# Optimization experiments

Measured on AMD Instinct MI355X. Metric: run time of the kernel, lower is better.

The kernel has to match this reference:

```python
import jax, jax.numpy as jnp
import numpy as np
import math

H = 16          # num_attention_heads
DH = 64         # attention_head_size
D = H * DH      # hidden_size
MAXPOS = 512    # max_position_embeddings
ALPHA = 12.0
MAX_SEQ = 512
GAMMA = -ALPHA / MAX_SEQ
ETA = 1.0


def setup_inputs() -> dict:
    key = jax.random.key(0)
    ks = jax.random.split(key, 10)
    B, S = 16, 512
    s = 1.0 / math.sqrt(D)
    return {
        "hidden_states": jax.random.normal(ks[0], (B, S, D), jnp.float32),
        "attention_mask": jnp.zeros((B, 1, 1, S), jnp.float32),
        "Wq": jax.random.normal(ks[1], (D, D), jnp.float32) * s,
        "bq": jnp.zeros((D,), jnp.float32),
        "Wk": jax.random.normal(ks[2], (D, D), jnp.float32) * s,
        "bk": jnp.zeros((D,), jnp.float32),
        "Wv": jax.random.normal(ks[3], (D, D), jnp.float32) * s,
        "bv": jnp.zeros((D,), jnp.float32),
        "dist_emb": jax.random.normal(ks[4], (2 * MAXPOS - 1, DH), jnp.float32) * 0.02,
        "gate_w": jax.random.normal(ks[5], (H, DH), jnp.float32) * 0.01,
        "gate_b": jnp.zeros((H,), jnp.float32),
    }


def _heads(x, B, S):
    # [B,S,D] -> [B,H,S,DH]
    return x.reshape(B, S, H, DH).transpose(0, 2, 1, 3)


def reference(hidden_states, attention_mask, Wq, bq, Wk, bk, Wv, bv,
              dist_emb, gate_w, gate_b):
    B, S, _ = hidden_states.shape
    q = _heads(hidden_states @ Wq + bq, B, S)  # bhsd
    k = _heads(hidden_states @ Wk + bk, B, S)
    v = _heads(hidden_states @ Wv + bv, B, S)

    scores = jnp.einsum("bhqd,bhkd->bhqk", q, k)

    # relative_key_query positional scores
    pos = jnp.arange(S)
    distance = pos[:, None] - pos[None, :]          # [S,S]
    pe = dist_emb[distance + MAXPOS - 1]            # [S,S,DH]
    scores = scores + jnp.einsum("bhld,lrd->bhlr", q, pe) \
                    + jnp.einsum("bhrd,lrd->bhlr", k, pe)

    scores = scores / math.sqrt(DH) + attention_mask

    # clipped softmax: clip((eta-gamma)*softmax(x) + gamma, 0, 1)
    probs = jnp.clip(jax.nn.softmax(scores, axis=-1) * (ETA - GAMMA) + GAMMA,
                     0.0, 1.0)

    ctx = jnp.einsum("bhqk,bhkd->bhqd", probs, v)

    # conditional_per_token per-head gate: sigmoid(Linear(head_dim -> 1))
    x_heads = _heads(hidden_states, B, S)            # bhsd
    gate = jax.nn.sigmoid(
        jnp.einsum("bhsd,hd->bhs", x_heads, gate_w) + gate_b[None, :, None])
    ctx = ctx * gate[..., None]

    return ctx.transpose(0, 2, 1, 3).reshape(B, S, D)
```

## Files before the change

kernel.cpp:

```cpp
#include <hip/hip_runtime.h>

typedef __attribute__((ext_vector_type(8))) short s16x8;
typedef __attribute__((ext_vector_type(4))) short s16x4;
typedef __attribute__((ext_vector_type(4))) float f32x4;

__device__ __forceinline__ f32x4 mfma16(s16x8 a, s16x8 b, f32x4 c) {
  return __builtin_amdgcn_mfma_f32_16x16x32_bf16(a, b, c, 0, 0, 0);
}
__device__ __forceinline__ f32x4 zero4() {
  f32x4 z = {0.f, 0.f, 0.f, 0.f};
  return z;
}

__device__ __forceinline__ unsigned short f2b(float f) {
  unsigned u = __float_as_uint(f);
  u = u + 0x7fffu + ((u >> 16) & 1u);
  return (unsigned short)(u >> 16);
}
__device__ __forceinline__ float b2f(unsigned short u) {
  return __uint_as_float(((unsigned)u) << 16);
}
__device__ __forceinline__ unsigned packbf(float a, float b) {
  return (unsigned)f2b(a) | ((unsigned)f2b(b) << 16);
}


__global__ __launch_bounds__(256) void k0a_convx_gate(
    const float* __restrict__ X, const float* __restrict__ gw,
    const float* __restrict__ gb, unsigned short* __restrict__ Xb,
    float* __restrict__ gate) {
  int row = blockIdx.x;
  int t = threadIdx.x;
  const float* xr = X + (size_t)row * 1024;
  float4 x = *(const float4*)(xr + t * 4);
  s16x4 o;
  o.x = (short)f2b(x.x); o.y = (short)f2b(x.y);
  o.z = (short)f2b(x.z); o.w = (short)f2b(x.w);
  *(s16x4*)(&Xb[(size_t)row * 1024 + t * 4]) = o;
  int h = t >> 4;
  int e0 = (t & 15) * 4;
  const float* g4 = gw + h * 64 + e0;
  float part = x.x * g4[0] + x.y * g4[1] + x.z * g4[2] + x.w * g4[3];
  part += __shfl_xor(part, 1);
  part += __shfl_xor(part, 2);
  part += __shfl_xor(part, 4);
  part += __shfl_xor(part, 8);
  if ((t & 15) == 0) {
    int b = row >> 9, s = row & 511;
    float z = part + gb[h];
    gate[((size_t)(b * 16 + h)) * 512 + s] = 1.0f / (1.0f + __expf(-z));
  }
}

__global__ __launch_bounds__(256) void k0b_wtrans(
    const float* __restrict__ Wq, const float* __restrict__ Wk,
    const float* __restrict__ Wv, unsigned short* __restrict__ Wt) {
  __shared__ float tile[64][68];
  int z = blockIdx.z;
  const float* W = (z == 0) ? Wq : (z == 1) ? Wk : Wv;
  unsigned short* O = Wt + (size_t)z * 1024 * 1024;
  int k0 = blockIdx.x * 64, n0 = blockIdx.y * 64;
  int t = threadIdx.x;
  int kl = t >> 4, nl = (t & 15) * 4;
#pragma unroll
  for (int p = 0; p < 4; ++p) {
    float4 v = *(const float4*)(W + (size_t)(k0 + p * 16 + kl) * 1024 + n0 + nl);
    tile[p * 16 + kl][nl + 0] = v.x;
    tile[p * 16 + kl][nl + 1] = v.y;
    tile[p * 16 + kl][nl + 2] = v.z;
    tile[p * 16 + kl][nl + 3] = v.w;
  }
  __syncthreads();
  for (int idx = t; idx < 4096; idx += 256) {
    int nl2 = idx >> 6, kl2 = idx & 63;
    O[(size_t)(n0 + nl2) * 1024 + k0 + kl2] = f2b(tile[kl2][nl2]);
  }
}

__global__ __launch_bounds__(256) void k0c_conve(const float* __restrict__ E,
                                                 unsigned short* __restrict__ Eb) {
  int idx = blockIdx.x * 256 + threadIdx.x;
  int row = idx >> 6;
  float v = (row < 1023) ? E[idx] : 0.0f;
  Eb[idx] = f2b(v);
}

__global__ __launch_bounds__(256) void k1_qkv(
    const unsigned short* __restrict__ Xb, const unsigned short* __restrict__ Wt,
    const float* __restrict__ bq, const float* __restrict__ bk,
    const float* __restrict__ bv, unsigned short* __restrict__ Qb,
    unsigned short* __restrict__ Kb, unsigned short* __restrict__ Vt) {
  __shared__ short As[128 * 72];
  __shared__ short Ws[128 * 72];
  int t = threadIdx.x;
  int wv = t >> 6, lane = t & 63, quad = lane >> 4, l15 = lane & 15;
  int wm = wv >> 1, wn = wv & 1;
  int m0 = blockIdx.x * 128, n0 = blockIdx.y * 128, z = blockIdx.z;
  const unsigned short* W = Wt + (size_t)z * 1024 * 1024;
  f32x4 acc[4][4];
#pragma unroll
  for (int i = 0; i < 4; ++i)
#pragma unroll
    for (int j = 0; j < 4; ++j) acc[i][j] = zero4();

  for (int kt = 0; kt < 16; ++kt) {
    int k0 = kt * 64;
    __syncthreads();
#pragma unroll
    for (int p = 0; p < 4; ++p) {
      int g = p * 256 + t;
      int row = g >> 3, cg = g & 7;
      int4 va = *(const int4*)(Xb + (size_t)(m0 + row) * 1024 + k0 + cg * 8);
      *(int4*)(&As[row * 72 + cg * 8]) = va;
      int4 vb = *(const int4*)(W + (size_t)(n0 + row) * 1024 + k0 + cg * 8);
      *(int4*)(&Ws[row * 72 + cg * 8]) = vb;
    }
    __syncthreads();
#pragma unroll
    for (int ks = 0; ks < 2; ++ks) {
      s16x8 a[4], bb[4];
#pragma unroll
      for (int i = 0; i < 4; ++i)
        a[i] = *(const s16x8*)(&As[(wm * 64 + i * 16 + l15) * 72 + ks * 32 + quad * 8]);
#pragma unroll
      for (int j = 0; j < 4; ++j)
        bb[j] = *(const s16x8*)(&Ws[(wn * 64 + j * 16 + l15) * 72 + ks * 32 + quad * 8]);
#pragma unroll
      for (int i = 0; i < 4; ++i)
#pragma unroll
        for (int j = 0; j < 4; ++j)
          acc[i][j] = mfma16(a[i], bb[j], acc[i][j]);
    }
  }
  const float* bias = (z == 0) ? bq : (z == 1) ? bk : bv;
#pragma unroll
  for (int i = 0; i < 4; ++i) {
    int mbase = m0 + wm * 64 + i * 16 + quad * 4;
#pragma unroll
    for (int j = 0; j < 4; ++j) {
      int n = n0 + wn * 64 + j * 16 + l15;
      float bvv = bias[n];
      int h = n >> 6, dh = n & 63;
#pragma unroll
      for (int r = 0; r < 4; ++r) {
        int m = mbase + r;
        int b = m >> 9, s = m & 511;
        unsigned short u = f2b(acc[i][j][r] + bvv);
        if (z == 2)
          Vt[(size_t)((b * 16 + h) * 64 + dh) * 512 + s] = u;
        else if (z == 0)
          Qb[(size_t)((b * 16 + h) * 512 + s) * 64 + dh] = u;
        else
          Kb[(size_t)((b * 16 + h) * 512 + s) * 64 + dh] = u;
      }
    }
  }
}

__global__ __launch_bounds__(256, 3) void k2_attn(
    const unsigned short* __restrict__ Qb, const unsigned short* __restrict__ Kb,
    const unsigned short* __restrict__ Vt, const unsigned short* __restrict__ Eb,
    const float* __restrict__ gate, const float* __restrict__ mask,
    float* __restrict__ out) {
  __shared__ short Ks[64 * 72];
  __shared__ short Ss1[128 * 68];
  __shared__ short Ss2[128 * 68];
  __shared__ short Ps[64 * 72];

  int t = threadIdx.x;
  int wv = t >> 6, lane = t & 63, quad = lane >> 4, l15 = lane & 15;
  int bid = blockIdx.x;
  int bh = bid >> 3, qt = bid & 7;
  int b = bh >> 4, hh = bh & 15;
  int l0 = qt * 64;

  int srow = t >> 3, scg = t & 7;

  s16x8 aq0, aq1;
  {
    const unsigned short* qp = Qb + ((size_t)bh * 512 + l0 + wv * 16 + l15) * 64 + quad * 8;
    aq0 = *(const s16x8*)(qp);
    aq1 = *(const s16x8*)(qp + 32);
  }

  float lsum[4];
#pragma unroll
  for (int r = 0; r < 4; ++r) lsum[r] = 0.0f;
  unsigned stash[64];

#pragma unroll
  for (int kt = 0; kt < 8; ++kt) {
    int r0 = kt * 64;
    int4 kv0 = *(const int4*)(Kb + ((size_t)bh * 512 + r0 + srow) * 64 + scg * 8);
    int4 kv1 = *(const int4*)(Kb + ((size_t)bh * 512 + r0 + srow + 32) * 64 + scg * 8);
    __syncthreads();
    *(int4*)(&Ks[srow * 72 + scg * 8]) = kv0;
    *(int4*)(&Ks[(srow + 32) * 72 + scg * 8]) = kv1;
    __syncthreads();
    s16x8 ak0 = *(const s16x8*)(&Ks[(wv * 16 + l15) * 72 + quad * 8]);
    s16x8 ak1 = *(const s16x8*)(&Ks[(wv * 16 + l15) * 72 + 32 + quad * 8]);
    int estart = (qt - kt) * 64 + 448;
#pragma unroll
    for (int nf = 0; nf < 8; ++nf) {
      const s16x8* ep = (const s16x8*)(Eb + (size_t)(estart + nf * 16 + l15) * 64 + quad * 8);
      s16x8 eb0 = ep[0];
      s16x8 eb1 = ep[4];
      f32x4 s1 = mfma16(aq1, eb1, mfma16(aq0, eb0, zero4()));
      s16x4 w1;
      w1.x = (short)f2b(s1[0]); w1.y = (short)f2b(s1[1]);
      w1.z = (short)f2b(s1[2]); w1.w = (short)f2b(s1[3]);
      *(s16x4*)(&Ss1[(nf * 16 + l15) * 68 + wv * 16 + quad * 4]) = w1;
      f32x4 s2 = mfma16(ak1, eb1, mfma16(ak0, eb0, zero4()));
      s16x4 w2;
      w2.x = (short)f2b(s2[0]); w2.y = (short)f2b(s2[1]);
      w2.z = (short)f2b(s2[2]); w2.w = (short)f2b(s2[3]);
      *(s16x4*)(&Ss2[(nf * 16 + l15) * 68 + wv * 16 + quad * 4]) = w2;
    }
    f32x4 s[4];
#pragma unroll
    for (int nf = 0; nf < 4; ++nf) {
      s16x8 b0 = *(const s16x8*)(&Ks[(nf * 16 + l15) * 72 + quad * 8]);
      s16x8 b1 = *(const s16x8*)(&Ks[(nf * 16 + l15) * 72 + 32 + quad * 8]);
      s[nf] = mfma16(aq1, b1, mfma16(aq0, b0, zero4()));
    }
    __syncthreads();
#pragma unroll
    for (int nf = 0; nf < 4; ++nf) {
      float mkv = mask[b * 512 + kt * 64 + nf * 16 + l15];
      int dr = nf * 16 + l15;
      float ex[4];
#pragma unroll
      for (int r = 0; r < 4; ++r) {
        int dl = wv * 16 + quad * 4 + r;
        int tt = dl - dr + 63;
        float p1 = b2f((unsigned short)Ss1[tt * 68 + dl]);
        float p2 = b2f((unsigned short)Ss2[tt * 68 + dr]);
        float x = (s[nf][r] + p1 + p2) * 0.125f + mkv;
        ex[r] = __expf(x);
        lsum[r] += ex[r];
      }
      stash[kt * 8 + nf * 2 + 0] = packbf(ex[0], ex[1]);
      stash[kt * 8 + nf * 2 + 1] = packbf(ex[2], ex[3]);
    }
  }

#pragma unroll
  for (int r = 0; r < 4; ++r) {
    lsum[r] += __shfl_xor(lsum[r], 1);
    lsum[r] += __shfl_xor(lsum[r], 2);
    lsum[r] += __shfl_xor(lsum[r], 4);
    lsum[r] += __shfl_xor(lsum[r], 8);
  }
  float f1[4];
#pragma unroll
  for (int r = 0; r < 4; ++r) f1[r] = 1.0234375f / lsum[r];
  const float c0 = -0.0234375f;

  f32x4 ctx[4];
#pragma unroll
  for (int nf = 0; nf < 4; ++nf) ctx[nf] = zero4();

#pragma unroll
  for (int kt = 0; kt < 8; ++kt) {
#pragma unroll
    for (int nf = 0; nf < 4; ++nf) {
      unsigned u0 = stash[kt * 8 + nf * 2 + 0];
      unsigned u1 = stash[kt * 8 + nf * 2 + 1];
      float e0 = b2f((unsigned short)(u0 & 0xffff));
      float e1 = b2f((unsigned short)(u0 >> 16));
      float e2 = b2f((unsigned short)(u1 & 0xffff));
      float e3 = b2f((unsigned short)(u1 >> 16));
      float p0 = fminf(fmaxf(e0 * f1[0] + c0, 0.0f), 1.0f);
      float p1 = fminf(fmaxf(e1 * f1[1] + c0, 0.0f), 1.0f);
      float p2 = fminf(fmaxf(e2 * f1[2] + c0, 0.0f), 1.0f);
      float p3 = fminf(fmaxf(e3 * f1[3] + c0, 0.0f), 1.0f);
      int rowb = wv * 16 + quad * 4;
      Ps[(rowb + 0) * 72 + nf * 16 + l15] = (short)f2b(p0);
      Ps[(rowb + 1) * 72 + nf * 16 + l15] = (short)f2b(p1);
      Ps[(rowb + 2) * 72 + nf * 16 + l15] = (short)f2b(p2);
      Ps[(rowb + 3) * 72 + nf * 16 + l15] = (short)f2b(p3);
    }
    s16x8 ap0 = *(const s16x8*)(&Ps[(wv * 16 + l15) * 72 + quad * 8]);
    s16x8 ap1 = *(const s16x8*)(&Ps[(wv * 16 + l15) * 72 + 32 + quad * 8]);
#pragma unroll
    for (int nf = 0; nf < 4; ++nf) {
      const s16x8* vp = (const s16x8*)(Vt + ((size_t)bh * 64 + nf * 16 + l15) * 512 + kt * 64 + quad * 8);
      s16x8 vb0 = vp[0];
      s16x8 vb1 = vp[4];
      ctx[nf] = mfma16(ap1, vb1, mfma16(ap0, vb0, ctx[nf]));
    }
  }

#pragma unroll
  for (int r = 0; r < 4; ++r) {
    int s = l0 + wv * 16 + quad * 4 + r;
    float g = gate[(size_t)bh * 512 + s];
#pragma unroll
    for (int nf = 0; nf < 4; ++nf)
      out[((size_t)(b * 512 + s)) * 1024 + hh * 64 + nf * 16 + l15] = ctx[nf][r] * g;
  }
}

extern "C" void kernel_launch(void* const* d_in, const int* in_sizes, int n_in,
                              void* d_out, int out_size, void* d_ws, size_t ws_size,
                              hipStream_t stream) {
  const float* X = (const float*)d_in[0];
  const float* mask = (const float*)d_in[1];
  const float* Wq = (const float*)d_in[2];
  const float* bq = (const float*)d_in[3];
  const float* Wk = (const float*)d_in[4];
  const float* bk = (const float*)d_in[5];
  const float* Wv = (const float*)d_in[6];
  const float* bv = (const float*)d_in[7];
  const float* dist = (const float*)d_in[8];
  const float* gw = (const float*)d_in[9];
  const float* gb = (const float*)d_in[10];
  float* out = (float*)d_out;

  char* ws = (char*)d_ws;
  constexpr size_t OFF_XB = 0;
  constexpr size_t OFF_WT = 16777216;
  constexpr size_t OFF_QB = OFF_WT + 6291456;
  constexpr size_t OFF_KB = OFF_QB + 16777216;
  constexpr size_t OFF_VT = OFF_KB + 16777216;
  constexpr size_t OFF_EB = OFF_VT + 16777216;
  constexpr size_t OFF_GA = OFF_EB + 131072;

  unsigned short* Xb = (unsigned short*)(ws + OFF_XB);
  unsigned short* Wt = (unsigned short*)(ws + OFF_WT);
  unsigned short* Qb = (unsigned short*)(ws + OFF_QB);
  unsigned short* Kb = (unsigned short*)(ws + OFF_KB);
  unsigned short* Vt = (unsigned short*)(ws + OFF_VT);
  unsigned short* Eb = (unsigned short*)(ws + OFF_EB);
  float* gate = (float*)(ws + OFF_GA);

  hipLaunchKernelGGL(k0a_convx_gate, dim3(8192), dim3(256), 0, stream, X, gw, gb, Xb, gate);
  hipLaunchKernelGGL(k0b_wtrans, dim3(16, 16, 3), dim3(256), 0, stream, Wq, Wk, Wv, Wt);
  hipLaunchKernelGGL(k0c_conve, dim3(256), dim3(256), 0, stream, dist, Eb);
  hipLaunchKernelGGL(k1_qkv, dim3(64, 8, 3), dim3(256), 0, stream,
                     Xb, Wt, bq, bk, bv, Qb, Kb, Vt);
  hipLaunchKernelGGL(k2_attn, dim3(2048), dim3(256), 0, stream,
                     Qb, Kb, Vt, Eb, gate, mask, out);
}
```

Measured before the change: 406.9 us.

## Use direct global-to-LDS loads in QKV GEMM and drop K staging in attention

Result: slower. 471.1 us (+15.8%).

```diff
diff --git a/kernel.cpp b/kernel.cpp
--- a/kernel.cpp
+++ b/kernel.cpp
@@ -22,6 +22,12 @@
 }
 __device__ __forceinline__ unsigned packbf(float a, float b) {
   return (unsigned)f2b(a) | ((unsigned)f2b(b) << 16);
+}
+
+__device__ __forceinline__ void gld16(const void* g, void* l) {
+  __builtin_amdgcn_global_load_lds(
+      (const __attribute__((address_space(1))) void*)g,
+      (__attribute__((address_space(3))) void*)l, 16, 0, 0);
 }
 
 
@@ -90,30 +96,31 @@
     const float* __restrict__ bq, const float* __restrict__ bk,
     const float* __restrict__ bv, unsigned short* __restrict__ Qb,
     unsigned short* __restrict__ Kb, unsigned short* __restrict__ Vt) {
-  __shared__ short As[128 * 72];
-  __shared__ short Ws[128 * 72];
+  __shared__ short As[128 * 64];
+  __shared__ short Ws[128 * 64];
   int t = threadIdx.x;
   int wv = t >> 6, lane = t & 63, quad = lane >> 4, l15 = lane & 15;
   int wm = wv >> 1, wn = wv & 1;
-  int m0 = blockIdx.x * 128, n0 = blockIdx.y * 128, z = blockIdx.z;
+  int bx = blockIdx.x;
+  bx = ((bx & 7) << 3) | (bx >> 3);
+  int m0 = bx * 128, n0 = blockIdx.y * 128, z = blockIdx.z;
   const unsigned short* W = Wt + (size_t)z * 1024 * 1024;
   f32x4 acc[4][4];
 #pragma unroll
   for (int i = 0; i < 4; ++i)
 #pragma unroll
     for (int j = 0; j < 4; ++j) acc[i][j] = zero4();
+
+  int srow = t >> 3, scg = t & 7;
 
   for (int kt = 0; kt < 16; ++kt) {
     int k0 = kt * 64;
     __syncthreads();
 #pragma unroll
     for (int p = 0; p < 4; ++p) {
-      int g = p * 256 + t;
-      int row = g >> 3, cg = g & 7;
-      int4 va = *(const int4*)(Xb + (size_t)(m0 + row) * 1024 + k0 + cg * 8);
-      *(int4*)(&As[row * 72 + cg * 8]) = va;
-      int4 vb = *(const int4*)(W + (size_t)(n0 + row) * 1024 + k0 + cg * 8);
-      *(int4*)(&Ws[row * 72 + cg * 8]) = vb;
+      int row = srow + p * 32;
+      gld16(Xb + (size_t)(m0 + row) * 1024 + k0 + scg * 8, &As[row * 64 + scg * 8]);
+      gld16(W + (size_t)(n0 + row) * 1024 + k0 + scg * 8, &Ws[row * 64 + scg * 8]);
     }
     __syncthreads();
 #pragma unroll
@@ -121,10 +128,10 @@
       s16x8 a[4], bb[4];
 #pragma unroll
       for (int i = 0; i < 4; ++i)
-        a[i] = *(const s16x8*)(&As[(wm * 64 + i * 16 + l15) * 72 + ks * 32 + quad * 8]);
+        a[i] = *(const s16x8*)(&As[(wm * 64 + i * 16 + l15) * 64 + ks * 32 + quad * 8]);
 #pragma unroll
       for (int j = 0; j < 4; ++j)
-        bb[j] = *(const s16x8*)(&Ws[(wn * 64 + j * 16 + l15) * 72 + ks * 32 + quad * 8]);
+        bb[j] = *(const s16x8*)(&Ws[(wn * 64 + j * 16 + l15) * 64 + ks * 32 + quad * 8]);
 #pragma unroll
       for (int i = 0; i < 4; ++i)
 #pragma unroll
@@ -157,24 +164,22 @@
   }
 }
 
-__global__ __launch_bounds__(256, 3) void k2_attn(
+__global__ __launch_bounds__(256, 4) void k2_attn(
     const unsigned short* __restrict__ Qb, const unsigned short* __restrict__ Kb,
     const unsigned short* __restrict__ Vt, const unsigned short* __restrict__ Eb,
     const float* __restrict__ gate, const float* __restrict__ mask,
     float* __restrict__ out) {
-  __shared__ short Ks[64 * 72];
   __shared__ short Ss1[128 * 68];
   __shared__ short Ss2[128 * 68];
-  __shared__ short Ps[64 * 72];
 
   int t = threadIdx.x;
   int wv = t >> 6, lane = t & 63, quad = lane >> 4, l15 = lane & 15;
-  int bid = blockIdx.x;
+  int bid = ((blockIdx.x & 7) << 8) | (blockIdx.x >> 3);
   int bh = bid >> 3, qt = bid & 7;
   int b = bh >> 4, hh = bh & 15;
   int l0 = qt * 64;
 
-  int srow = t >> 3, scg = t & 7;
+  const unsigned short* Kbh = Kb + (size_t)bh * 512 * 64;
 
   s16x8 aq0, aq1;
   {
@@ -191,37 +196,32 @@
 #pragma unroll
   for (int kt = 0; kt < 8; ++kt) {
     int r0 = kt * 64;
-    int4 kv0 = *(const int4*)(Kb + ((size_t)bh * 512 + r0 + srow) * 64 + scg * 8);
-    int4 kv1 = *(const int4*)(Kb + ((size_t)bh * 512 + r0 + srow + 32) * 64 + scg * 8);
+    f32x4 s[4];
+#pragma unroll
+    for (int nf = 0; nf < 4; ++nf) {
+      const s16x8* kp = (const s16x8*)(Kbh + (size_t)(r0 + nf * 16 + l15) * 64 + quad * 8);
+      s16x8 kb0 = kp[0];
+      s16x8 kb1 = kp[4];
+      s[nf] = mfma16(aq1, kb1, mfma16(aq0, kb0, zero4()));
+    }
+    const unsigned short* kpr = Kbh + (size_t)(r0 + wv * 16 + l15) * 64 + quad * 8;
+    s16x8 ak0 = *(const s16x8*)(kpr);
+    s16x8 ak1 = *(const s16x8*)(kpr + 32);
+    int estart = (qt - kt) * 64 + 448;
     __syncthreads();
-    *(int4*)(&Ks[srow * 72 + scg * 8]) = kv0;
-    *(int4*)(&Ks[(srow + 32) * 72 + scg * 8]) = kv1;
-    __syncthreads();
-    s16x8 ak0 = *(const s16x8*)(&Ks[(wv * 16 + l15) * 72 + quad * 8]);
-    s16x8 ak1 = *(const s16x8*)(&Ks[(wv * 16 + l15) * 72 + 32 + quad * 8]);
-    int estart = (qt - kt) * 64 + 448;
 #pragma unroll
     for (int nf = 0; nf < 8; ++nf) {
       const s16x8* ep = (const s16x8*)(Eb + (size_t)(estart + nf * 16 + l15) * 64 + quad * 8);
       s16x8 eb0 = ep[0];
       s16x8 eb1 = ep[4];
       f32x4 s1 = mfma16(aq1, eb1, mfma16(aq0, eb0, zero4()));
-      s16x4 w1;
-      w1.x = (short)f2b(s1[0]); w1.y = (short)f2b(s1[1]);
-      w1.z = (short)f2b(s1[2]); w1.w = (short)f2b(s1[3]);
-      *(s16x4*)(&Ss1[(nf * 16 + l15) * 68 + wv * 16 + quad * 4]) = w1;
+      unsigned* w1 = (unsigned*)(&Ss1[(nf * 16 + l15) * 68 + wv * 16 + quad * 4]);
+      w1[0] = packbf(s1[0], s1[1]);
+      w1[1] = packbf(s1[2], s1[3]);
       f32x4 s2 = mfma16(ak1, eb1, mfma16(ak0, eb0, zero4()));
-      s16x4 w2;
-      w2.x = (short)f2b(s2[0]); w2.y = (short)f2b(s2[1]);
-      w2.z = (short)f2b(s2[2]); w2.w = (short)f2b(s2[3]);
-      *(s16x4*)(&Ss2[(nf * 16 + l15) * 68 + wv * 16 + quad * 4]) = w2;
-    }
-    f32x4 s[4];
-#pragma unroll
-    for (int nf = 0; nf < 4; ++nf) {
-      s16x8 b0 = *(const s16x8*)(&Ks[(nf * 16 + l15) * 72 + quad * 8]);
-      s16x8 b1 = *(const s16x8*)(&Ks[(nf * 16 + l15) * 72 + 32 + quad * 8]);
-      s[nf] = mfma16(aq1, b1, mfma16(aq0, b0, zero4()));
+      unsigned* w2 = (unsigned*)(&Ss2[(nf * 16 + l15) * 68 + wv * 16 + quad * 4]);
+      w2[0] = packbf(s2[0], s2[1]);
+      w2[1] = packbf(s2[2], s2[3]);
     }
     __syncthreads();
 #pragma unroll
@@ -256,12 +256,16 @@
   for (int r = 0; r < 4; ++r) f1[r] = 1.0234375f / lsum[r];
   const float c0 = -0.0234375f;
 
+  __syncthreads();
+  short* Ps = Ss1;
+
   f32x4 ctx[4];
 #pragma unroll
   for (int nf = 0; nf < 4; ++nf) ctx[nf] = zero4();
 
 #pragma unroll
   for (int kt = 0; kt < 8; ++kt) {
+    int rowb = wv * 16 + quad * 4;
 #pragma unroll
     for (int nf = 0; nf < 4; ++nf) {
       unsigned u0 = stash[kt * 8 + nf * 2 + 0];
@@ -274,7 +278,6 @@
       float p1 = fminf(fmaxf(e1 * f1[1] + c0, 0.0f), 1.0f);
       float p2 = fminf(fmaxf(e2 * f1[2] + c0, 0.0f), 1.0f);
       float p3 = fminf(fmaxf(e3 * f1[3] + c0, 0.0f), 1.0f);
-      int rowb = wv * 16 + quad * 4;
       Ps[(rowb + 0) * 72 + nf * 16 + l15] = (short)f2b(p0);
       Ps[(rowb + 1) * 72 + nf * 16 + l15] = (short)f2b(p1);
       Ps[(rowb + 2) * 72 + nf * 16 + l15] = (short)f2b(p2);
```
